# Optimization experiments

Measured on AMD Instinct MI355X. Metric: run time of the kernel, lower is better.

The kernel has to match this reference:

```python
import jax, jax.numpy as jnp
import numpy as np

DIM = 768
NUM_HEADS = 12
HEAD_DIM = DIM // NUM_HEADS
SCALE = HEAD_DIM ** -0.5


def setup_inputs() -> dict:
    key = jax.random.key(0)
    k1, k2, k3, k4 = jax.random.split(key, 4)
    B, H, W = 8, 32, 32
    x = jax.random.normal(k1, (B, H, W, DIM), dtype=jnp.float32)
    s = DIM ** -0.5
    w_qkv = jax.random.normal(k2, (DIM, 3 * DIM), dtype=jnp.float32) * s
    w_proj = jax.random.normal(k3, (DIM, DIM), dtype=jnp.float32) * s
    b_proj = jax.random.normal(k4, (DIM,), dtype=jnp.float32) * 0.01
    return {"x": x, "w_qkv": w_qkv, "w_proj": w_proj, "b_proj": b_proj}


def reference(x, w_qkv, w_proj, b_proj):
    B, H, W, C = x.shape
    N = H * W
    qkv = (x.reshape(B, N, C) @ w_qkv).reshape(B, N, 3, NUM_HEADS, HEAD_DIM)
    q, k, v = jnp.moveaxis(qkv, 2, 0)  # each (B, N, h, d)
    # scores: (B, h, N, N)
    attn = jnp.einsum('bnhd,bmhd->bhnm', q * SCALE, k)
    attn = jax.nn.softmax(attn, axis=-1)
    out = jnp.einsum('bhnm,bmhd->bnhd', attn, v).reshape(B, H, W, C)
    return out @ w_proj + b_proj
```

## Files before the change

### kernel.cpp

```cpp
#include <hip/hip_runtime.h>

typedef _Float16 half_t;
typedef __attribute__((ext_vector_type(4))) _Float16 half4;
typedef __attribute__((ext_vector_type(8))) _Float16 half8;
typedef __attribute__((ext_vector_type(4))) float floatx4;

#define MFMA_F16(A,B,C)  __builtin_amdgcn_mfma_f32_16x16x32_f16(A,B,C,0,0,0)

typedef __attribute__((address_space(1))) const void gvoid_t;
typedef __attribute__((address_space(3))) void svoid_t;

__device__ __forceinline__ void async_copy16(const half_t* g, half_t* l) {
    __builtin_amdgcn_global_load_lds((gvoid_t*)g, (svoid_t*)l, 16, 0, 0);
}

__global__ __launch_bounds__(256)
void prep_kernel(const float* __restrict__ x, const float* __restrict__ w_qkv,
                 const float* __restrict__ w_proj, half_t* __restrict__ xh,
                 half_t* __restrict__ wqkvT, half_t* __restrict__ wprojT)
{
    __shared__ half_t tile[64 * 65];
    const int id = blockIdx.x, tid = threadIdx.x;
    if (id < 6144) {
        size_t e = (size_t)id * 1024 + tid * 4;
        float4 f = *(const float4*)(x + e);
        half4 h = { (half_t)f.x, (half_t)f.y, (half_t)f.z, (half_t)f.w };
        *(half4*)(xh + e) = h;
        return;
    }
    const float* src; half_t* dst; int lds, tr0, tc0;
    if (id < 6576) { int t = id - 6144; src = w_qkv; dst = wqkvT; lds = 2304;
                     tr0 = (t / 36) * 64; tc0 = (t % 36) * 64; }
    else           { int t = id - 6576; src = w_proj; dst = wprojT; lds = 768;
                     tr0 = (t / 12) * 64; tc0 = (t % 12) * 64; }
    #pragma unroll
    for (int i = 0; i < 4; i++) {
        int e = tid + i * 256, r = e >> 4, c4 = (e & 15) << 2;
        float4 f = *(const float4*)(src + (size_t)(tr0 + r) * lds + tc0 + c4);
        tile[(c4 + 0) * 65 + r] = (half_t)f.x;
        tile[(c4 + 1) * 65 + r] = (half_t)f.y;
        tile[(c4 + 2) * 65 + r] = (half_t)f.z;
        tile[(c4 + 3) * 65 + r] = (half_t)f.w;
    }
    __syncthreads();
    #pragma unroll
    for (int i = 0; i < 4; i++) {
        int e = tid + i * 256, c = e >> 4, r4 = (e & 15) << 2;
        half4 h = { tile[c * 65 + r4], tile[c * 65 + r4 + 1],
                    tile[c * 65 + r4 + 2], tile[c * 65 + r4 + 3] };
        *(half4*)(dst + (size_t)(tc0 + c) * 768 + tr0 + r4) = h;
    }
}

__global__ __launch_bounds__(256, 2)
void gemm_qkv(const half_t* __restrict__ A, const half_t* __restrict__ Bt,
              half_t* __restrict__ q_ws, half_t* __restrict__ k_ws,
              half_t* __restrict__ v_ws)
{
    __shared__ half_t As[128 * 64];
    __shared__ half_t Bs[256 * 64];

    const int lin  = blockIdx.x;
    const int xcd  = lin & 7, rest = lin >> 3;
    const int m0 = ((rest / 9) * 8 + xcd) * 128;
    const int n0 = (rest % 9) * 256;

    const int tid  = threadIdx.x;
    const int lane = tid & 63;
    const int w    = tid >> 6;
    const int quad = lane >> 4, l16 = lane & 15;
    const int lrow = lane >> 3;
    const int lcc  = (lane & 7) ^ lrow;
    const int xsw  = l16 & 7;

    const half_t* Ag = A  + (size_t)(m0 + w * 32 + lrow) * 768 + lcc * 8;
    const half_t* Bg = Bt + (size_t)(n0 + w * 64 + lrow) * 768 + lcc * 8;

    floatx4 acc[8][4];
    #pragma unroll
    for (int i = 0; i < 8; i++)
        #pragma unroll
        for (int j = 0; j < 4; j++) acc[i][j] = (floatx4)0.0f;

    for (int k0 = 0; k0 < 768; k0 += 64) {
        #pragma unroll
        for (int i = 0; i < 4; i++)
            async_copy16(Ag + (size_t)(i * 8) * 768 + k0, As + (w * 4 + i) * 512);
        #pragma unroll
        for (int i = 0; i < 8; i++)
            async_copy16(Bg + (size_t)(i * 8) * 768 + k0, Bs + (w * 8 + i) * 512);
        __syncthreads();

        #pragma unroll
        for (int ks = 0; ks < 2; ks++) {
            const int co = (((ks << 2) + quad) ^ xsw) * 8;
            half8 a[8], b[4];
            #pragma unroll
            for (int mi = 0; mi < 8; mi++)
                a[mi] = *(const half8*)(As + (mi * 16 + l16) * 64 + co);
            #pragma unroll
            for (int ni = 0; ni < 4; ni++)
                b[ni] = *(const half8*)(Bs + (w * 64 + ni * 16 + l16) * 64 + co);
            #pragma unroll
            for (int mi = 0; mi < 8; mi++)
                #pragma unroll
                for (int ni = 0; ni < 4; ni++)
                    acc[mi][ni] = MFMA_F16(a[mi], b[ni], acc[mi][ni]);
        }
        __syncthreads();
    }

    const int sel  = n0 / 768;
    const int rem0 = n0 - sel * 768;
    #pragma unroll
    for (int mi = 0; mi < 8; mi++) {
        #pragma unroll
        for (int ni = 0; ni < 4; ni++) {
            int gnr = rem0 + w * 64 + ni * 16 + l16;
            int h = gnr >> 6, d = gnr & 63;
            #pragma unroll
            for (int r = 0; r < 4; r++) {
                int gm = m0 + mi * 16 + quad * 4 + r;
                int bb = gm >> 10, tok = gm & 1023;
                size_t base = (size_t)(bb * 12 + h) * 65536;
                float val = acc[mi][ni][r];
                if (sel == 0)      q_ws[base + (size_t)tok * 64 + d] = (half_t)(val * 0.125f);
                else if (sel == 1) k_ws[base + (size_t)tok * 64 + d] = (half_t)val;
                else {
                    int tokp = (tok & ~31) | (quad << 3) | ((mi & 1) << 2) | r;
                    v_ws[base + (size_t)d * 1024 + tokp] = (half_t)val;
                }
            }
        }
    }
}

__global__ __launch_bounds__(256, 2)
void gemm_proj(const half_t* __restrict__ A, const half_t* __restrict__ Bt,
               float* __restrict__ Cout, const float* __restrict__ bias)
{
    __shared__ half_t As[128 * 64];
    __shared__ half_t Bs[128 * 64];

    const int lin  = blockIdx.x;
    const int xcd  = lin & 7, rest = lin >> 3;
    const int m0 = ((rest / 6) * 8 + xcd) * 128;
    const int n0 = (rest % 6) * 128;

    const int tid  = threadIdx.x;
    const int lane = tid & 63;
    const int w    = tid >> 6;
    const int wm   = w >> 1, wn = w & 1;
    const int quad = lane >> 4, l16 = lane & 15;
    const int lrow = lane >> 3;
    const int lcc  = (lane & 7) ^ lrow;
    const int xsw  = l16 & 7;

    const half_t* Ag = A  + (size_t)(m0 + w * 32 + lrow) * 768 + lcc * 8;
    const half_t* Bg = Bt + (size_t)(n0 + w * 32 + lrow) * 768 + lcc * 8;

    floatx4 acc[4][4];
    #pragma unroll
    for (int i = 0; i < 4; i++)
        #pragma unroll
        for (int j = 0; j < 4; j++) acc[i][j] = (floatx4)0.0f;

    for (int k0 = 0; k0 < 768; k0 += 64) {
        #pragma unroll
        for (int i = 0; i < 4; i++) {
            async_copy16(Ag + (size_t)(i * 8) * 768 + k0, As + (w * 4 + i) * 512);
            async_copy16(Bg + (size_t)(i * 8) * 768 + k0, Bs + (w * 4 + i) * 512);
        }
        __syncthreads();

        #pragma unroll
        for (int ks = 0; ks < 2; ks++) {
            const int co = (((ks << 2) + quad) ^ xsw) * 8;
            half8 a[4], b[4];
            #pragma unroll
            for (int mi = 0; mi < 4; mi++)
                a[mi] = *(const half8*)(As + (wm * 64 + mi * 16 + l16) * 64 + co);
            #pragma unroll
            for (int ni = 0; ni < 4; ni++)
                b[ni] = *(const half8*)(Bs + (wn * 64 + ni * 16 + l16) * 64 + co);
            #pragma unroll
            for (int mi = 0; mi < 4; mi++)
                #pragma unroll
                for (int ni = 0; ni < 4; ni++)
                    acc[mi][ni] = MFMA_F16(a[mi], b[ni], acc[mi][ni]);
        }
        __syncthreads();
    }

    #pragma unroll
    for (int mi = 0; mi < 4; mi++)
        #pragma unroll
        for (int ni = 0; ni < 4; ni++) {
            int gn = n0 + wn * 64 + ni * 16 + l16;
            #pragma unroll
            for (int r = 0; r < 4; r++) {
                int gm = m0 + wm * 64 + mi * 16 + quad * 4 + r;
                Cout[(size_t)gm * 768 + gn] = acc[mi][ni][r] + bias[gn];
            }
        }
}

__global__ __launch_bounds__(256, 3)
void attn_kernel(const half_t* __restrict__ q, const half_t* __restrict__ k,
                 const half_t* __restrict__ vT, half_t* __restrict__ a_ws)
{
    __shared__ __align__(16) half_t Kb[2][4096];
    __shared__ __align__(16) half_t Vb[2][4096];

    const int lin  = blockIdx.x;
    const int xcd  = lin & 7, rest = lin >> 3;
    const int qc   = rest & 7;
    const int bh   = (rest >> 3) * 8 + xcd;

    const int tid  = threadIdx.x;
    const int lane = tid & 63;
    const int w    = tid >> 6;
    const int quad = lane >> 4, l16 = lane & 15;

    const half_t* kg = k  + (size_t)bh * 65536;
    const half_t* vg = vT + (size_t)bh * 65536;

    const int srow = lane >> 3;
    const int sch  = (lane & 7) ^ srow;

    const half_t* qp = q + ((size_t)bh * 1024 + qc * 128 + w * 16 + l16) * 64;
    half8 qf[2][2];
    #pragma unroll
    for (int T = 0; T < 2; T++)
        #pragma unroll
        for (int ks = 0; ks < 2; ks++)
            qf[T][ks] = *(const half8*)(qp + T * 4096 + ks * 32 + quad * 8);

    floatx4 acc_o[2][4];
    floatx4 lacc[2];
    #pragma unroll
    for (int T = 0; T < 2; T++) {
        lacc[T] = (floatx4)0.0f;
        #pragma unroll
        for (int dt = 0; dt < 4; dt++) acc_o[T][dt] = (floatx4)0.0f;
    }

    const int xsw = l16 & 7;
    const half8 vone = { (half_t)1.0f, (half_t)1.0f, (half_t)1.0f, (half_t)1.0f,
                         (half_t)1.0f, (half_t)1.0f, (half_t)1.0f, (half_t)1.0f };

    #pragma unroll
    for (int j = 0; j < 2; j++) {
        int row = j * 32 + w * 8;
        async_copy16(kg + (size_t)(row + srow) * 64 + sch * 8, &Kb[0][row * 64]);
        async_copy16(vg + (size_t)(row + srow) * 1024 + sch * 8, &Vb[0][row * 64]);
    }

    for (int kt = 0; kt < 16; kt++) {
        const int cb = kt & 1;
        __syncthreads();
        if (kt < 15) {
            #pragma unroll
            for (int j = 0; j < 2; j++) {
                int row = j * 32 + w * 8;
                async_copy16(kg + (size_t)((kt + 1) * 64 + row + srow) * 64 + sch * 8,
                             &Kb[cb ^ 1][row * 64]);
                async_copy16(vg + (size_t)(row + srow) * 1024 + (kt + 1) * 64 + sch * 8,
                             &Vb[cb ^ 1][row * 64]);
            }
        }
        const half_t* Kc = Kb[cb];
        const half_t* Vc = Vb[cb];

        floatx4 sc[2][4];
        #pragma unroll
        for (int T = 0; T < 2; T++)
            #pragma unroll
            for (int mt = 0; mt < 4; mt++) sc[T][mt] = (floatx4)0.0f;
        #pragma unroll
        for (int ks = 0; ks < 2; ks++)
            #pragma unroll
            for (int mt = 0; mt < 4; mt++) {
                half8 kf = *(const half8*)(Kc + (mt * 16 + l16) * 64
                                              + (((ks << 2) + quad) ^ xsw) * 8);
                sc[0][mt] = MFMA_F16(kf, qf[0][ks], sc[0][mt]);
                sc[1][mt] = MFMA_F16(kf, qf[1][ks], sc[1][mt]);
            }

        half8 pa[2][2];
        #pragma unroll
        for (int T = 0; T < 2; T++)
            #pragma unroll
            for (int g = 0; g < 2; g++) {
                half8 ph;
                #pragma unroll
                for (int r = 0; r < 4; r++) ph[r]     = (half_t)__expf(sc[T][2 * g][r]);
                #pragma unroll
                for (int r = 0; r < 4; r++) ph[4 + r] = (half_t)__expf(sc[T][2 * g + 1][r]);
                pa[T][g] = ph;
            }

        #pragma unroll
        for (int g = 0; g < 2; g++) {
            lacc[0] = MFMA_F16(pa[0][g], vone, lacc[0]);
            lacc[1] = MFMA_F16(pa[1][g], vone, lacc[1]);
            #pragma unroll
            for (int dt = 0; dt < 4; dt++) {
                half8 vb = *(const half8*)(Vc + (dt * 16 + l16) * 64
                                              + ((((g << 2) + quad) ^ xsw) << 3));
                acc_o[0][dt] = MFMA_F16(pa[0][g], vb, acc_o[0][dt]);
                acc_o[1][dt] = MFMA_F16(pa[1][g], vb, acc_o[1][dt]);
            }
        }
    }

    const int b = bh / 12, h = bh - (bh / 12) * 12;
    #pragma unroll
    for (int T = 0; T < 2; T++)
        #pragma unroll
        for (int r = 0; r < 4; r++) {
            float inv = 1.0f / lacc[T][r];
            int n = qc * 128 + T * 64 + w * 16 + quad * 4 + r;
            half_t* op = a_ws + ((size_t)(b * 1024 + n)) * 768 + h * 64;
            #pragma unroll
            for (int dt = 0; dt < 4; dt++)
                op[dt * 16 + l16] = (half_t)(acc_o[T][dt][r] * inv);
        }
}

extern "C" void kernel_launch(void* const* d_in, const int* in_sizes, int n_in,
                              void* d_out, int out_size, void* d_ws, size_t ws_size,
                              hipStream_t stream)
{
    (void)in_sizes; (void)n_in; (void)out_size; (void)ws_size;
    const float* x      = (const float*)d_in[0];
    const float* w_qkv  = (const float*)d_in[1];
    const float* w_proj = (const float*)d_in[2];
    const float* b_proj = (const float*)d_in[3];
    float* out = (float*)d_out;

    half_t* ws     = (half_t*)d_ws;
    half_t* q_ws   = ws;
    half_t* k_ws   = ws + 6291456;
    half_t* v_ws   = ws + 2 * 6291456;
    half_t* xh     = ws + 3 * 6291456;
    half_t* wqkvT  = ws + 4 * 6291456;
    half_t* wprojT = wqkvT + 1769472;
    half_t* a_ws   = xh;

    prep_kernel<<<dim3(6720), dim3(256), 0, stream>>>(x, w_qkv, w_proj, xh, wqkvT, wprojT);
    gemm_qkv<<<dim3(576), dim3(256), 0, stream>>>(xh, wqkvT, q_ws, k_ws, v_ws);
    attn_kernel<<<dim3(768), dim3(256), 0, stream>>>(q_ws, k_ws, v_ws, a_ws);
    gemm_proj<<<dim3(384), dim3(256), 0, stream>>>(a_ws, wprojT, out, b_proj);
}
```

Before: 194.6 us.

## Vectorize QKV/proj epilogue stores and stage transposed Q through LDS

The QKV GEMM epilogue now writes Q in a transposed (d-major) layout and writes Q and V as half4 vector stores instead of scalar half stores. The projection GEMM epilogue stages accumulator tiles plus bias through shared-memory scratch so each row is written to global memory as contiguous float4 stores. The attention kernel reads transposed Q tiles into LDS with async copies and gathers its fragments there. The aim is to cut uncoalesced, scattered global stores, at the cost of extra LDS traffic, an added barrier and strided scalar LDS reads for Q.

```diff
diff --git a/kernel.cpp b/kernel.cpp
--- a/kernel.cpp
+++ b/kernel.cpp
@@ -112,26 +112,48 @@
 
     const int sel  = n0 / 768;
     const int rem0 = n0 - sel * 768;
-    #pragma unroll
-    for (int mi = 0; mi < 8; mi++) {
-        #pragma unroll
-        for (int ni = 0; ni < 4; ni++) {
-            int gnr = rem0 + w * 64 + ni * 16 + l16;
-            int h = gnr >> 6, d = gnr & 63;
-            #pragma unroll
-            for (int r = 0; r < 4; r++) {
-                int gm = m0 + mi * 16 + quad * 4 + r;
-                int bb = gm >> 10, tok = gm & 1023;
-                size_t base = (size_t)(bb * 12 + h) * 65536;
-                float val = acc[mi][ni][r];
-                if (sel == 0)      q_ws[base + (size_t)tok * 64 + d] = (half_t)(val * 0.125f);
-                else if (sel == 1) k_ws[base + (size_t)tok * 64 + d] = (half_t)val;
-                else {
-                    int tokp = (tok & ~31) | (quad << 3) | ((mi & 1) << 2) | r;
-                    v_ws[base + (size_t)d * 1024 + tokp] = (half_t)val;
+    const int hh   = (rem0 >> 6) + w;
+    const int bb   = m0 >> 10;
+    const int t0   = m0 & 1023;
+    const size_t base = (size_t)(bb * 12 + hh) * 65536;
+
+    if (sel == 0) {
+        #pragma unroll
+        for (int mi = 0; mi < 8; mi++)
+            #pragma unroll
+            for (int ni = 0; ni < 4; ni++) {
+                int d   = ni * 16 + l16;
+                int tok = t0 + mi * 16 + quad * 4;
+                half4 hv = { (half_t)(acc[mi][ni][0] * 0.125f),
+                             (half_t)(acc[mi][ni][1] * 0.125f),
+                             (half_t)(acc[mi][ni][2] * 0.125f),
+                             (half_t)(acc[mi][ni][3] * 0.125f) };
+                *(half4*)(q_ws + base + (size_t)d * 1024 + tok) = hv;
+            }
+    } else if (sel == 1) {
+        #pragma unroll
+        for (int mi = 0; mi < 8; mi++)
+            #pragma unroll
+            for (int ni = 0; ni < 4; ni++) {
+                int d = ni * 16 + l16;
+                #pragma unroll
+                for (int r = 0; r < 4; r++) {
+                    int tok = t0 + mi * 16 + quad * 4 + r;
+                    k_ws[base + (size_t)tok * 64 + d] = (half_t)acc[mi][ni][r];
                 }
             }
-        }
+    } else {
+        #pragma unroll
+        for (int mi = 0; mi < 8; mi++)
+            #pragma unroll
+            for (int ni = 0; ni < 4; ni++) {
+                int d    = ni * 16 + l16;
+                int tokb = (t0 + mi * 16 + quad * 4) & ~31;
+                int tokp = tokb | (quad << 3) | ((mi & 1) << 2);
+                half4 hv = { (half_t)acc[mi][ni][0], (half_t)acc[mi][ni][1],
+                             (half_t)acc[mi][ni][2], (half_t)acc[mi][ni][3] };
+                *(half4*)(v_ws + base + (size_t)d * 1024 + tokp) = hv;
+            }
     }
 }
 
@@ -192,25 +214,36 @@
         __syncthreads();
     }
 
-    #pragma unroll
-    for (int mi = 0; mi < 4; mi++)
-        #pragma unroll
-        for (int ni = 0; ni < 4; ni++) {
-            int gn = n0 + wn * 64 + ni * 16 + l16;
-            #pragma unroll
-            for (int r = 0; r < 4; r++) {
-                int gm = m0 + wm * 64 + mi * 16 + quad * 4 + r;
-                Cout[(size_t)gm * 768 + gn] = acc[mi][ni][r] + bias[gn];
-            }
-        }
+    float bias_v[4];
+    #pragma unroll
+    for (int ni = 0; ni < 4; ni++)
+        bias_v[ni] = bias[n0 + wn * 64 + ni * 16 + l16];
+    float* scratch = (w < 2 ? (float*)As : (float*)Bs) + (w & 1) * 1152;
+    #pragma unroll
+    for (int mi = 0; mi < 4; mi++) {
+        #pragma unroll
+        for (int ni = 0; ni < 4; ni++)
+            #pragma unroll
+            for (int r = 0; r < 4; r++)
+                scratch[(quad * 4 + r) * 72 + ni * 16 + l16] =
+                    acc[mi][ni][r] + bias_v[ni];
+        #pragma unroll
+        for (int i = 0; i < 4; i++) {
+            int f = quad + i * 4;
+            float4 v4 = *(const float4*)(scratch + l16 * 72 + f * 4);
+            int gm = m0 + wm * 64 + mi * 16 + l16;
+            *(float4*)(Cout + (size_t)gm * 768 + n0 + wn * 64 + f * 4) = v4;
+        }
+    }
 }
 
 __global__ __launch_bounds__(256, 3)
-void attn_kernel(const half_t* __restrict__ q, const half_t* __restrict__ k,
+void attn_kernel(const half_t* __restrict__ qT, const half_t* __restrict__ k,
                  const half_t* __restrict__ vT, half_t* __restrict__ a_ws)
 {
     __shared__ __align__(16) half_t Kb[2][4096];
     __shared__ __align__(16) half_t Vb[2][4096];
+    __shared__ __align__(16) half_t Qs[64 * 128];
 
     const int lin  = blockIdx.x;
     const int xcd  = lin & 7, rest = lin >> 3;
@@ -222,39 +255,49 @@
     const int w    = tid >> 6;
     const int quad = lane >> 4, l16 = lane & 15;
 
+    const half_t* qg = qT + (size_t)bh * 65536;
     const half_t* kg = k  + (size_t)bh * 65536;
     const half_t* vg = vT + (size_t)bh * 65536;
 
     const int srow = lane >> 3;
     const int sch  = (lane & 7) ^ srow;
 
-    const half_t* qp = q + ((size_t)bh * 1024 + qc * 128 + w * 16 + l16) * 64;
-    half8 qf[2][2];
-    #pragma unroll
-    for (int T = 0; T < 2; T++)
-        #pragma unroll
-        for (int ks = 0; ks < 2; ks++)
-            qf[T][ks] = *(const half8*)(qp + T * 4096 + ks * 32 + quad * 8);
-
-    floatx4 acc_o[2][4];
-    floatx4 lacc[2];
-    #pragma unroll
-    for (int T = 0; T < 2; T++) {
-        lacc[T] = (floatx4)0.0f;
-        #pragma unroll
-        for (int dt = 0; dt < 4; dt++) acc_o[T][dt] = (floatx4)0.0f;
-    }
-
-    const int xsw = l16 & 7;
-    const half8 vone = { (half_t)1.0f, (half_t)1.0f, (half_t)1.0f, (half_t)1.0f,
-                         (half_t)1.0f, (half_t)1.0f, (half_t)1.0f, (half_t)1.0f };
-
+    #pragma unroll
+    for (int j = 0; j < 4; j++) {
+        int d0 = w * 16 + j * 4;
+        async_copy16(qg + (size_t)(d0 + (lane >> 4)) * 1024 + qc * 128 + (lane & 15) * 8,
+                     &Qs[d0 * 128]);
+    }
     #pragma unroll
     for (int j = 0; j < 2; j++) {
         int row = j * 32 + w * 8;
         async_copy16(kg + (size_t)(row + srow) * 64 + sch * 8, &Kb[0][row * 64]);
         async_copy16(vg + (size_t)(row + srow) * 1024 + sch * 8, &Vb[0][row * 64]);
     }
+    __syncthreads();
+
+    half8 qf[2][2];
+    #pragma unroll
+    for (int T = 0; T < 2; T++)
+        #pragma unroll
+        for (int ks = 0; ks < 2; ks++)
+            #pragma unroll
+            for (int j = 0; j < 8; j++)
+                qf[T][ks][j] = Qs[(ks * 32 + quad * 8 + j) * 128
+                                  + T * 64 + w * 16 + l16];
+
+    floatx4 acc_o[2][4];
+    floatx4 lacc[2];
+    #pragma unroll
+    for (int T = 0; T < 2; T++) {
+        lacc[T] = (floatx4)0.0f;
+        #pragma unroll
+        for (int dt = 0; dt < 4; dt++) acc_o[T][dt] = (floatx4)0.0f;
+    }
+
+    const int xsw = l16 & 7;
+    const half8 vone = { (half_t)1.0f, (half_t)1.0f, (half_t)1.0f, (half_t)1.0f,
+                         (half_t)1.0f, (half_t)1.0f, (half_t)1.0f, (half_t)1.0f };
 
     for (int kt = 0; kt < 16; kt++) {
         const int cb = kt & 1;
```

After: 183.9 us. 1.06x faster.
